# Optimization experiments

Measured on AMD Instinct MI355X. Metric: run time of the kernel, lower is better.

The kernel has to match this reference:

```python
import jax, jax.numpy as jnp
import numpy as np

N, E, B = 20000, 160000, 64
NFEAT, NHID, HEADS, NCLASS = 128, 64, 16, 10
GAT_SLOPE = 0.2    # LeakyReLU inside GATv2 attention
OUT_SLOPE = 0.01   # torch.nn.functional.leaky_relu default
TEMPERATURE = 1.0


def _lrelu(x, slope):
    return jnp.where(x >= 0, x, slope * x)


def gatv2_conv(x, src, dst, Wl, bl, Wr, br, att, bias):
    # x: [N, Fin]; PyG GATv2Conv with share_weights=False, concat=False (mean over heads)
    xl = (x @ Wl + bl).reshape(N, HEADS, NHID)   # source-side transform
    xr = (x @ Wr + br).reshape(N, HEADS, NHID)   # target-side transform
    e = _lrelu(xl[src] + xr[dst], GAT_SLOPE)     # [E', H, C] per-edge pre-activation
    logit = jnp.einsum('ehc,hc->eh', e, att)     # [E', H]
    # segment softmax over incoming edges of each target node (self-loops guarantee >=1 edge)
    m = jax.ops.segment_max(logit, dst, num_segments=N)
    m = jnp.where(jnp.isfinite(m), m, 0.0)
    ex = jnp.exp(logit - m[dst])
    den = jax.ops.segment_sum(ex, dst, num_segments=N)
    alpha = ex / den[dst]                        # [E', H]
    out = jax.ops.segment_sum(alpha[:, :, None] * xl[src], dst, num_segments=N)  # [N, H, C]
    return out.mean(axis=1) + bias               # concat=False -> head average, then bias


def setup_inputs() -> dict:
    key = jax.random.key(0)
    ks = jax.random.split(key, 20)
    s = 0.05
    inp = {
        'x': jax.random.normal(ks[0], (N, NFEAT), dtype=jnp.float32),
        'edge_index': jax.random.randint(ks[1], (2, E), 0, N, dtype=jnp.int64)
            if jax.config.jax_enable_x64 else jax.random.randint(ks[1], (2, E), 0, N).astype(jnp.int32),
        'batch': jnp.sort(jax.random.randint(ks[2], (N,), 0, B)).astype(jnp.int32),
        # GATv2 layer 1
        'W1l': jax.random.normal(ks[3], (NFEAT, HEADS * NHID), dtype=jnp.float32) * s,
        'b1l': jnp.zeros((HEADS * NHID,), jnp.float32),
        'W1r': jax.random.normal(ks[4], (NFEAT, HEADS * NHID), dtype=jnp.float32) * s,
        'b1r': jnp.zeros((HEADS * NHID,), jnp.float32),
        'att1': jax.random.normal(ks[5], (HEADS, NHID), dtype=jnp.float32) * s,
        'bias1': jnp.zeros((NHID,), jnp.float32),
        # GATv2 layer 2
        'W2l': jax.random.normal(ks[6], (NHID, HEADS * NHID), dtype=jnp.float32) * s,
        'b2l': jnp.zeros((HEADS * NHID,), jnp.float32),
        'W2r': jax.random.normal(ks[7], (NHID, HEADS * NHID), dtype=jnp.float32) * s,
        'b2r': jnp.zeros((HEADS * NHID,), jnp.float32),
        'att2': jax.random.normal(ks[8], (HEADS, NHID), dtype=jnp.float32) * s,
        'bias2': jnp.zeros((NHID,), jnp.float32),
        # heads
        'Wc': jax.random.normal(ks[9], (NHID, NCLASS), dtype=jnp.float32) * s,
        'bc': jnp.zeros((NCLASS,), jnp.float32),
        'Wv': jax.random.normal(ks[10], (NHID, 1), dtype=jnp.float32) * s,
        'bv': jnp.zeros((1,), jnp.float32),
    }
    return inp


def reference(x, edge_index, batch, W1l, b1l, W1r, b1r, att1, bias1,
              W2l, b2l, W2r, b2r, att2, bias2, Wc, bc, Wv, bv):
    loop = jnp.arange(N, dtype=edge_index.dtype)  # PyG add_self_loops=True
    src = jnp.concatenate([edge_index[0], loop])
    dst = jnp.concatenate([edge_index[1], loop])

    h = _lrelu(gatv2_conv(x, src, dst, W1l, b1l, W1r, b1r, att1, bias1), OUT_SLOPE)
    h = _lrelu(gatv2_conv(h, src, dst, W2l, b2l, W2r, b2r, att2, bias2), OUT_SLOPE)
    # dropout p=0.0 -> identity

    sums = jax.ops.segment_sum(h, batch, num_segments=B)           # [B, NHID]
    cnt = jax.ops.segment_sum(jnp.ones((N,), h.dtype), batch, num_segments=B)
    pooled = sums / jnp.maximum(cnt, 1.0)[:, None]                 # global_mean_pool

    logits = (pooled @ Wc + bc) / TEMPERATURE                      # [B, NCLASS]
    log_var = pooled @ Wv + bv                                     # [B, 1]
    return (logits, log_var)
```

## Files before the change

### kernel.cpp

```cpp
#include <hip/hip_runtime.h>
#include <hip/hip_bf16.h>
#include <hip/hip_fp16.h>
#include <math.h>

#define NN   20000
#define EE   160000
#define NBAT 64
#define NF   128
#define NH   64
#define NHEAD 16
#define NCLS 10
#define ETOT (EE + NN)

#define SCAN_BLK 1024
#define SCAN_NB  ((NN + SCAN_BLK - 1) / SCAN_BLK)

typedef __attribute__((ext_vector_type(8))) _Float16 half8;
typedef __attribute__((ext_vector_type(2))) _Float16 h2v;
typedef __attribute__((ext_vector_type(4))) float f32x4;
typedef unsigned short ushort_t;

#if __has_builtin(__builtin_amdgcn_fdot2)
typedef __fp16 fdot2_t __attribute__((ext_vector_type(2)));
static __device__ __forceinline__ float dot2(h2v a, h2v b, float c) {
    return __builtin_amdgcn_fdot2(__builtin_bit_cast(fdot2_t, a),
                                  __builtin_bit_cast(fdot2_t, b), c, false);
}
#else
static __device__ __forceinline__ float dot2(h2v a, h2v b, float c) {
    return c + (float)a.x * (float)b.x + (float)a.y * (float)b.y;
}
#endif

__global__ void k_hist_bounds(const int* __restrict__ ei, int* __restrict__ deg,
                              const int* __restrict__ batch, int* __restrict__ bstart) {
    int g = blockIdx.x * 256 + threadIdx.x;
    if (g < EE) atomicAdd(&deg[ei[EE + g]], 1);
    if (g < NN) {
        int b = batch[g];
        if (g == 0) for (int bb = 0; bb <= b; ++bb) bstart[bb] = 0;
        int bn = (g + 1 < NN) ? batch[g + 1] : NBAT;
        for (int bb = b + 1; bb <= bn; ++bb) bstart[bb] = g + 1;
    }
}

__global__ void k_scanA(const int* __restrict__ deg, int* __restrict__ incl,
                        int* __restrict__ bsum) {
    __shared__ int sh[SCAN_BLK];
    int t = threadIdx.x, idx = blockIdx.x * SCAN_BLK + t;
    int v = (idx < NN) ? deg[idx] : 0;
    sh[t] = v;
    __syncthreads();
    for (int off = 1; off < SCAN_BLK; off <<= 1) {
        int u = (t >= off) ? sh[t - off] : 0;
        __syncthreads();
        sh[t] += u;
        __syncthreads();
    }
    incl[idx] = sh[t];
    if (t == SCAN_BLK - 1) bsum[blockIdx.x] = sh[t];
}

__global__ void k_scanB(const int* __restrict__ bsum, int* __restrict__ boff,
                        int* __restrict__ rowptr) {
    if (threadIdx.x == 0) {
        int acc = 0;
        for (int b = 0; b < SCAN_NB; ++b) { boff[b] = acc; acc += bsum[b]; }
        rowptr[NN] = acc + NN;
    }
}

__global__ void k_scanC(const int* __restrict__ deg, const int* __restrict__ incl,
                        const int* __restrict__ boff, int* __restrict__ rowptr,
                        int* __restrict__ cursor, int* __restrict__ csr) {
    int idx = blockIdx.x * 256 + threadIdx.x;
    if (idx >= NN) return;
    int b = idx >> 10;
    int excl = boff[b] + incl[idx] - deg[idx];
    int base = excl + idx;
    rowptr[idx] = base;
    csr[base]   = idx;
    cursor[idx] = base + 1;
}

__global__ void k_scatter(const int* __restrict__ ei, int* __restrict__ cursor,
                          int* __restrict__ csr) {
    int e = blockIdx.x * 256 + threadIdx.x;
    if (e >= EE) return;
    int s = ei[e], d = ei[EE + e];
    int pos = atomicAdd(&cursor[d], 1);
    csr[pos] = s;
}

__global__ void k_split_w4(
    const float* __restrict__ W0, _Float16* __restrict__ T0,
    const float* __restrict__ W1, _Float16* __restrict__ T1,
    const float* __restrict__ W2, _Float16* __restrict__ T2,
    const float* __restrict__ W3, _Float16* __restrict__ T3)
{
    const int z = blockIdx.y;
    const float* W; _Float16* T; int K;
    if      (z == 0) { W = W0; T = T0; K = NF; }
    else if (z == 1) { W = W1; T = T1; K = NF; }
    else if (z == 2) { W = W2; T = T2; K = NH; }
    else             { W = W3; T = T3; K = NH; }
    int idx = blockIdx.x * 256 + threadIdx.x;
    if (idx >= K * 1024) return;
    int k = idx >> 10, n = idx & 1023;
    T[n * K + k] = (_Float16)W[idx];
}


template<int K>
__global__ __launch_bounds__(256) void k_gemm_l1(
    const float* __restrict__ X, int M,
    const _Float16* __restrict__ Wt0, const float* __restrict__ b0, _Float16* __restrict__ O0,
    const _Float16* __restrict__ Wt1, const float* __restrict__ b1, _Float16* __restrict__ O1)
{
    const _Float16* Wt = blockIdx.z ? Wt1 : Wt0;
    const float*    bi = blockIdx.z ? b1 : b0;
    _Float16*       O  = blockIdx.z ? O1 : O0;

    const int r0 = blockIdx.x * 128;
    const int c0 = blockIdx.y * 128;

    __shared__ __align__(16) ushort_t SH[128 * 128];
    char* AsB = (char*)SH;
    char* WsB = (char*)SH + 16384;

    const int t = threadIdx.x;
    const int lane = t & 63;
    const int wv = t >> 6, wr = wv >> 1, wc = wv & 1;
    const int fr = lane & 15;
    const int k0 = (lane >> 4) * 8;

    f32x4 acc[4][4] = {};

    for (int kt = 0; kt < K; kt += 64) {
        #pragma unroll
        for (int p = 0; p < 4; ++p) {
            int idx = p * 256 + t;
            int m  = idx >> 3;
            int kc = (idx & 7) * 8;
            int gr = r0 + m;
            half8 hv = {};
            if (gr < M) {
                float4 v0 = *(const float4*)(X + (size_t)gr * K + kt + kc);
                float4 v1 = *(const float4*)(X + (size_t)gr * K + kt + kc + 4);
                hv[0] = (_Float16)v0.x; hv[1] = (_Float16)v0.y;
                hv[2] = (_Float16)v0.z; hv[3] = (_Float16)v0.w;
                hv[4] = (_Float16)v1.x; hv[5] = (_Float16)v1.y;
                hv[6] = (_Float16)v1.z; hv[7] = (_Float16)v1.w;
            }
            int sw = (m * 128 + kc * 2) ^ ((m & 7) << 4);
            *(uint4*)(AsB + sw) = __builtin_bit_cast(uint4, hv);
            uint4 wv4 = *(const uint4*)(Wt + (size_t)(c0 + m) * K + kt + kc);
            *(uint4*)(WsB + sw) = wv4;
        }
        __syncthreads();

        #pragma unroll
        for (int ks = 0; ks < 64; ks += 32) {
            half8 a[4], b[4];
            #pragma unroll
            for (int i = 0; i < 4; ++i) {
                int row = wr * 64 + i * 16 + fr;
                int off = (row * 128 + (ks + k0) * 2) ^ ((row & 7) << 4);
                a[i] = *(const half8*)(AsB + off);
            }
            #pragma unroll
            for (int j = 0; j < 4; ++j) {
                int col = wc * 64 + j * 16 + fr;
                int off = (col * 128 + (ks + k0) * 2) ^ ((col & 7) << 4);
                b[j] = *(const half8*)(WsB + off);
            }
            #pragma unroll
            for (int i = 0; i < 4; ++i)
                #pragma unroll
                for (int j = 0; j < 4; ++j)
                    acc[i][j] = __builtin_amdgcn_mfma_f32_16x16x32_f16(a[i], b[j], acc[i][j], 0, 0, 0);
        }
        __syncthreads();
    }

    float bj[4];
    #pragma unroll
    for (int j = 0; j < 4; ++j) bj[j] = bi[c0 + wc * 64 + j * 16 + fr];
    #pragma unroll
    for (int i = 0; i < 4; ++i) {
        #pragma unroll
        for (int r = 0; r < 4; ++r) {
            int row_l = wr * 64 + i * 16 + (lane >> 4) * 4 + r;
            int s = ((row_l >> 2) & 7) << 4;
            #pragma unroll
            for (int j = 0; j < 4; ++j) {
                int col_l = wc * 64 + j * 16 + fr;
                *(_Float16*)((char*)SH + ((row_l * 256 + col_l * 2) ^ s)) =
                    (_Float16)(acc[i][j][r] + bj[j]);
            }
        }
    }
    __syncthreads();
    #pragma unroll
    for (int it = 0; it < 8; ++it) {
        int idx = it * 256 + t;
        int row_l = idx >> 4, c16 = idx & 15;
        int gr = r0 + row_l;
        if (gr < M) {
            int s = ((row_l >> 2) & 7) << 4;
            uint4 v = *(const uint4*)((char*)SH + ((row_l * 256 + c16 * 16) ^ s));
            *(uint4*)(O + (size_t)gr * 1024 + c0 + c16 * 8) = v;
        }
    }
}

template<int K>
__global__ __launch_bounds__(256) void k_gemm_l2(
    const _Float16* __restrict__ A, int M,
    const _Float16* __restrict__ Wt0, const float* __restrict__ b0, _Float16* __restrict__ O0,
    const _Float16* __restrict__ Wt1, const float* __restrict__ b1, _Float16* __restrict__ O1)
{
    const _Float16* Wt = blockIdx.z ? Wt1 : Wt0;
    const float*    bi = blockIdx.z ? b1 : b0;
    _Float16*       O  = blockIdx.z ? O1 : O0;

    const int r0 = blockIdx.x * 128;
    const int c0 = blockIdx.y * 128;

    __shared__ __align__(16) ushort_t SH[128 * 128];
    char* AsB = (char*)SH;
    char* WsB = (char*)SH + 16384;

    const int t = threadIdx.x;
    const int lane = t & 63;
    const int wv = t >> 6, wr = wv >> 1, wc = wv & 1;
    const int fr = lane & 15;
    const int k0 = (lane >> 4) * 8;

    f32x4 acc[4][4] = {};

    #pragma unroll
    for (int p = 0; p < 4; ++p) {
        int idx = p * 256 + t;
        int m  = idx >> 3;
        int kc = (idx & 7) * 8;
        int gr = r0 + m;
        uint4 av = make_uint4(0, 0, 0, 0);
        if (gr < M) av = *(const uint4*)(A + (size_t)gr * K + kc);
        int sw = (m * 128 + kc * 2) ^ ((m & 7) << 4);
        *(uint4*)(AsB + sw) = av;
        uint4 wv4 = *(const uint4*)(Wt + (size_t)(c0 + m) * K + kc);
        *(uint4*)(WsB + sw) = wv4;
    }
    __syncthreads();

    #pragma unroll
    for (int ks = 0; ks < 64; ks += 32) {
        half8 a[4], b[4];
        #pragma unroll
        for (int i = 0; i < 4; ++i) {
            int row = wr * 64 + i * 16 + fr;
            int off = (row * 128 + (ks + k0) * 2) ^ ((row & 7) << 4);
            a[i] = *(const half8*)(AsB + off);
        }
        #pragma unroll
        for (int j = 0; j < 4; ++j) {
            int col = wc * 64 + j * 16 + fr;
            int off = (col * 128 + (ks + k0) * 2) ^ ((col & 7) << 4);
            b[j] = *(const half8*)(WsB + off);
        }
        #pragma unroll
        for (int i = 0; i < 4; ++i)
            #pragma unroll
            for (int j = 0; j < 4; ++j)
                acc[i][j] = __builtin_amdgcn_mfma_f32_16x16x32_f16(a[i], b[j], acc[i][j], 0, 0, 0);
    }
    __syncthreads();

    float bj[4];
    #pragma unroll
    for (int j = 0; j < 4; ++j) bj[j] = bi[c0 + wc * 64 + j * 16 + fr];
    #pragma unroll
    for (int i = 0; i < 4; ++i) {
        #pragma unroll
        for (int r = 0; r < 4; ++r) {
            int row_l = wr * 64 + i * 16 + (lane >> 4) * 4 + r;
            int s = ((row_l >> 2) & 7) << 4;
            #pragma unroll
            for (int j = 0; j < 4; ++j) {
                int col_l = wc * 64 + j * 16 + fr;
                *(_Float16*)((char*)SH + ((row_l * 256 + col_l * 2) ^ s)) =
                    (_Float16)(acc[i][j][r] + bj[j]);
            }
        }
    }
    __syncthreads();
    #pragma unroll
    for (int it = 0; it < 8; ++it) {
        int idx = it * 256 + t;
        int row_l = idx >> 4, c16 = idx & 15;
        int gr = r0 + row_l;
        if (gr < M) {
            int s = ((row_l >> 2) & 7) << 4;
            uint4 v = *(const uint4*)((char*)SH + ((row_l * 256 + c16 * 16) ^ s));
            *(uint4*)(O + (size_t)gr * 1024 + c0 + c16 * 8) = v;
        }
    }
}

static __device__ __forceinline__ float logit8(
    half8 a0, half8 a1, half8 xr0, half8 xr1, const h2v* att2)
{
    half8 t0 = a0 + xr0;
    half8 t1 = a1 + xr1;
    t0 = __builtin_elementwise_max(t0, t0 * (_Float16)0.2f);
    t1 = __builtin_elementwise_max(t1, t1 * (_Float16)0.2f);
    const h2v* p0 = (const h2v*)&t0;
    const h2v* p1 = (const h2v*)&t1;
    float lg = 0.f;
    #pragma unroll
    for (int j = 0; j < 4; ++j) lg = dot2(p0[j], att2[j], lg);
    #pragma unroll
    for (int j = 0; j < 4; ++j) lg = dot2(p1[j], att2[4 + j], lg);
    return lg;
}

__global__ __launch_bounds__(256) void k_attn(
    const _Float16* __restrict__ xl, const _Float16* __restrict__ xr,
    const float* __restrict__ att, const float* __restrict__ bias,
    const int* __restrict__ rowptr, const int* __restrict__ csr,
    _Float16* __restrict__ hout)
{
    const int wave = threadIdx.x >> 6;
    const int lane = threadIdx.x & 63;
    const int n = blockIdx.x * 4 + wave;
    if (n >= NN) return;
    const int h  = lane >> 2;
    const int cc = lane & 3;
    const int cb = h * NH + cc * 16;

    h2v att2[8];
    #pragma unroll
    for (int i = 0; i < 4; ++i) {
        float4 a = *(const float4*)(att + cb + i * 4);
        att2[i * 2 + 0] = h2v{(_Float16)a.x, (_Float16)a.y};
        att2[i * 2 + 1] = h2v{(_Float16)a.z, (_Float16)a.w};
    }
    const half8 xr0 = *(const half8*)(xr + (size_t)n * 1024 + cb);
    const half8 xr1 = *(const half8*)(xr + (size_t)n * 1024 + cb + 8);

    float acc[16];
    #pragma unroll
    for (int j = 0; j < 16; ++j) acc[j] = 0.f;
    float den = 0.f;

    const int e0 = rowptr[n], e1 = rowptr[n + 1];
    for (int e = e0; e < e1; e += 4) {
        int src[4];
        #pragma unroll
        for (int j = 0; j < 4; ++j) {
            int ee = e + j;
            src[j] = csr[(ee < e1) ? ee : (e1 - 1)];
        }
        half8 xa0[4], xa1[4];
        #pragma unroll
        for (int j = 0; j < 4; ++j) {
            const _Float16* p = xl + (size_t)src[j] * 1024 + cb;
            xa0[j] = *(const half8*)p;
            xa1[j] = *(const half8*)(p + 8);
        }
        #pragma unroll
        for (int j = 0; j < 4; ++j) {
            float lg = logit8(xa0[j], xa1[j], xr0, xr1, att2);
            lg += __shfl_xor(lg, 1);
            lg += __shfl_xor(lg, 2);
            float p = (e + j < e1) ? __expf(lg) : 0.f;
            den += p;
            const _Float16* va = (const _Float16*)&xa0[j];
            const _Float16* vb = (const _Float16*)&xa1[j];
            #pragma unroll
            for (int q = 0; q < 8; ++q) acc[q]     = fmaf((float)va[q], p, acc[q]);
            #pragma unroll
            for (int q = 0; q < 8; ++q) acc[8 + q] = fmaf((float)vb[q], p, acc[8 + q]);
        }
    }

    const float inv = 1.f / den;
    float v[16];
    #pragma unroll
    for (int j = 0; j < 16; ++j) v[j] = acc[j] * inv;
    #pragma unroll
    for (int mask = 4; mask <= 32; mask <<= 1)
        #pragma unroll
        for (int j = 0; j < 16; ++j) v[j] += __shfl_xor(v[j], mask);

    if (h == 0) {
        float bvv[16];
        #pragma unroll
        for (int i = 0; i < 4; ++i)
            *(float4*)(bvv + i * 4) = *(const float4*)(bias + cc * 16 + i * 4);
        half8 o0, o1;
        #pragma unroll
        for (int j = 0; j < 8; ++j) {
            float t0 = v[j] * 0.0625f + bvv[j];
            float t1 = v[8 + j] * 0.0625f + bvv[8 + j];
            o0[j] = (_Float16)fmaxf(t0, 0.01f * t0);
            o1[j] = (_Float16)fmaxf(t1, 0.01f * t1);
        }
        *(half8*)(hout + (size_t)n * NH + cc * 16)     = o0;
        *(half8*)(hout + (size_t)n * NH + cc * 16 + 8) = o1;
    }
}

__global__ __launch_bounds__(256) void k_pool_heads(
    const _Float16* __restrict__ h2buf, const int* __restrict__ bstart,
    const float* __restrict__ Wc, const float* __restrict__ bc,
    const float* __restrict__ Wv, const float* __restrict__ bv,
    float* __restrict__ out)
{
    const int b = blockIdx.x;
    const int c = threadIdx.x & 63, r = threadIdx.x >> 6;
    const int s = bstart[b], e = bstart[b + 1];
    float sum = 0.f;
    for (int n = s + r; n < e; n += 4)
        sum += (float)h2buf[(size_t)n * NH + c];
    __shared__ float red[4][NH];
    red[r][c] = sum;
    __syncthreads();
    if (r == 0)
        red[0][c] = (red[0][c] + red[1][c] + red[2][c] + red[3][c]) /
                    fmaxf((float)(e - s), 1.f);
    __syncthreads();
    if (threadIdx.x < NCLS) {
        float a = bc[threadIdx.x];
        for (int k = 0; k < NH; ++k) a = fmaf(red[0][k], Wc[k * NCLS + threadIdx.x], a);
        out[b * NCLS + threadIdx.x] = a;
    } else if (threadIdx.x == NCLS) {
        float a = bv[0];
        for (int k = 0; k < NH; ++k) a = fmaf(red[0][k], Wv[k], a);
        out[NBAT * NCLS + b] = a;
    }
}

extern "C" void kernel_launch(void* const* d_in, const int* in_sizes, int n_in,
                              void* d_out, int out_size, void* d_ws, size_t ws_size,
                              hipStream_t stream)
{
    const float* x     = (const float*)d_in[0];
    const int*   ei    = (const int*)  d_in[1];
    const int*   batch = (const int*)  d_in[2];
    const float* W1l = (const float*)d_in[3],  *b1l = (const float*)d_in[4];
    const float* W1r = (const float*)d_in[5],  *b1r = (const float*)d_in[6];
    const float* att1 = (const float*)d_in[7], *bias1 = (const float*)d_in[8];
    const float* W2l = (const float*)d_in[9],  *b2l = (const float*)d_in[10];
    const float* W2r = (const float*)d_in[11], *b2r = (const float*)d_in[12];
    const float* att2 = (const float*)d_in[13], *bias2 = (const float*)d_in[14];
    const float* Wc = (const float*)d_in[15],  *bc = (const float*)d_in[16];
    const float* Wv = (const float*)d_in[17],  *bv = (const float*)d_in[18];
    float* out = (float*)d_out;

    char* ws = (char*)d_ws;
    size_t off = 0;
    auto carve = [&](size_t bytes) {
        char* p = ws + off;
        off = (off + bytes + 255) & ~(size_t)255;
        return p;
    };
    _Float16* xl    = (_Float16*)carve((size_t)NN * 1024 * 2);
    _Float16* xr    = (_Float16*)carve((size_t)NN * 1024 * 2);
    _Float16* h2f   = (_Float16*)carve((size_t)NN * NH * 2);
    _Float16* h1    = (_Float16*)carve((size_t)NN * NH * 2);
    _Float16* Wt1l  = (_Float16*)carve((size_t)1024 * NF * 2);
    _Float16* Wt1r  = (_Float16*)carve((size_t)1024 * NF * 2);
    _Float16* Wt2l  = (_Float16*)carve((size_t)1024 * NH * 2);
    _Float16* Wt2r  = (_Float16*)carve((size_t)1024 * NH * 2);
    int*      deg    = (int*)carve((size_t)NN * 4);
    int*      incl   = (int*)carve((size_t)SCAN_NB * SCAN_BLK * 4);
    int*      bsum   = (int*)carve((size_t)SCAN_NB * 4);
    int*      boff   = (int*)carve((size_t)SCAN_NB * 4);
    int*      cursor = (int*)carve((size_t)NN * 4);
    int*      rowptr = (int*)carve((size_t)(NN + 1) * 4);
    int*      csr    = (int*)carve((size_t)ETOT * 4);
    int*      bstart = (int*)carve((size_t)(NBAT + 1) * 4);

    hipMemsetAsync(deg, 0, (size_t)NN * 4, stream);

    k_hist_bounds<<<(EE + 255) / 256, 256, 0, stream>>>(ei, deg, batch, bstart);
    k_scanA<<<SCAN_NB, SCAN_BLK, 0, stream>>>(deg, incl, bsum);
    k_scanB<<<1, 64, 0, stream>>>(bsum, boff, rowptr);
    k_scanC<<<(NN + 255) / 256, 256, 0, stream>>>(deg, incl, boff, rowptr, cursor, csr);
    k_scatter<<<(EE + 255) / 256, 256, 0, stream>>>(ei, cursor, csr);

    k_split_w4<<<dim3((NF * 1024 + 255) / 256, 4), 256, 0, stream>>>(
        W1l, Wt1l, W1r, Wt1r, W2l, Wt2l, W2r, Wt2r);

    const int MB = (NN + 127) / 128;
    k_gemm_l1<NF><<<dim3(MB, 8, 2), 256, 0, stream>>>(
        x, NN, Wt1l, b1l, xl, Wt1r, b1r, xr);
    k_attn<<<NN / 4, 256, 0, stream>>>(xl, xr, att1, bias1, rowptr, csr, h1);
    k_gemm_l2<NH><<<dim3(MB, 8, 2), 256, 0, stream>>>(
        h1, NN, Wt2l, b2l, xl, Wt2r, b2r, xr);
    k_attn<<<NN / 4, 256, 0, stream>>>(xl, xr, att2, bias2, rowptr, csr, h2f);
    k_pool_heads<<<NBAT, 256, 0, stream>>>(h2f, bstart, Wc, bc, Wv, bv, out);
}
```

Before: 333.3 us.

## Fuse CSR build preprocessing into fewer kernels with atomic block offsets

Merges the degree histogram, batch bounds, and weight transpose/convert into one launch. The three-kernel scan becomes a single scan kernel that takes each block's base from a global atomic counter, so CSR segments can land in arbitrary block order. Attention now reads a row start plus degree instead of rowptr and runs 1024-thread blocks with 16 nodes each. This cuts several tiny launches and serial dependencies, but gives up the ordered CSR layout, which may hurt locality, and the larger blocks may change occupancy.

```diff
diff --git a/kernel.cpp b/kernel.cpp
--- a/kernel.cpp
+++ b/kernel.cpp
@@ -12,8 +12,10 @@
 #define NCLS 10
 #define ETOT (EE + NN)
 
-#define SCAN_BLK 1024
-#define SCAN_NB  ((NN + SCAN_BLK - 1) / SCAN_BLK)
+#define P2_BLK 1024
+#define P2_NB  ((NN + P2_BLK - 1) / P2_BLK)
+#define WELEMS (2 * NF * 1024 + 2 * NH * 1024)
+#define PRE1_TOT (EE + NN + WELEMS)
 
 typedef __attribute__((ext_vector_type(8))) _Float16 half8;
 typedef __attribute__((ext_vector_type(2))) _Float16 h2v;
@@ -32,55 +34,65 @@
 }
 #endif
 
-__global__ void k_hist_bounds(const int* __restrict__ ei, int* __restrict__ deg,
-                              const int* __restrict__ batch, int* __restrict__ bstart) {
+__global__ void k_pre1(
+    const int* __restrict__ ei, int* __restrict__ deg,
+    const int* __restrict__ batch, int* __restrict__ bstart,
+    const float* __restrict__ W1l, _Float16* __restrict__ Wt1l,
+    const float* __restrict__ W1r, _Float16* __restrict__ Wt1r,
+    const float* __restrict__ W2l, _Float16* __restrict__ Wt2l,
+    const float* __restrict__ W2r, _Float16* __restrict__ Wt2r)
+{
     int g = blockIdx.x * 256 + threadIdx.x;
-    if (g < EE) atomicAdd(&deg[ei[EE + g]], 1);
-    if (g < NN) {
-        int b = batch[g];
-        if (g == 0) for (int bb = 0; bb <= b; ++bb) bstart[bb] = 0;
-        int bn = (g + 1 < NN) ? batch[g + 1] : NBAT;
-        for (int bb = b + 1; bb <= bn; ++bb) bstart[bb] = g + 1;
-    }
-}
-
-__global__ void k_scanA(const int* __restrict__ deg, int* __restrict__ incl,
-                        int* __restrict__ bsum) {
-    __shared__ int sh[SCAN_BLK];
-    int t = threadIdx.x, idx = blockIdx.x * SCAN_BLK + t;
-    int v = (idx < NN) ? deg[idx] : 0;
-    sh[t] = v;
-    __syncthreads();
-    for (int off = 1; off < SCAN_BLK; off <<= 1) {
+    if (g < EE) {
+        atomicAdd(&deg[ei[EE + g]], 1);
+    } else if (g < EE + NN) {
+        int n = g - EE;
+        int b = batch[n];
+        if (n == 0) for (int bb = 0; bb <= b; ++bb) bstart[bb] = 0;
+        int bn = (n + 1 < NN) ? batch[n + 1] : NBAT;
+        for (int bb = b + 1; bb <= bn; ++bb) bstart[bb] = n + 1;
+    } else if (g < PRE1_TOT) {
+        int w = g - (EE + NN);
+        const float* W; _Float16* T; int K, local;
+        if      (w < NF * 1024)            { W = W1l; T = Wt1l; K = NF; local = w; }
+        else if (w < 2 * NF * 1024)        { W = W1r; T = Wt1r; K = NF; local = w - NF * 1024; }
+        else if (w < 2 * NF * 1024 + NH * 1024)
+                                           { W = W2l; T = Wt2l; K = NH; local = w - 2 * NF * 1024; }
+        else                               { W = W2r; T = Wt2r; K = NH; local = w - 2 * NF * 1024 - NH * 1024; }
+        int k = local >> 10, n = local & 1023;
+        T[n * K + k] = (_Float16)W[local];
+    }
+}
+
+__global__ __launch_bounds__(1024) void k_pre2(
+    const int* __restrict__ deg, int* __restrict__ gcur,
+    int* __restrict__ rowstart, int* __restrict__ cursor, int* __restrict__ csr)
+{
+    __shared__ int sh[P2_BLK];
+    __shared__ int base_sh;
+    int t = threadIdx.x;
+    int idx = blockIdx.x * P2_BLK + t;
+    int d = (idx < NN) ? deg[idx] : 0;
+    sh[t] = d;
+    __syncthreads();
+    for (int off = 1; off < P2_BLK; off <<= 1) {
         int u = (t >= off) ? sh[t - off] : 0;
         __syncthreads();
         sh[t] += u;
         __syncthreads();
     }
-    incl[idx] = sh[t];
-    if (t == SCAN_BLK - 1) bsum[blockIdx.x] = sh[t];
-}
-
-__global__ void k_scanB(const int* __restrict__ bsum, int* __restrict__ boff,
-                        int* __restrict__ rowptr) {
-    if (threadIdx.x == 0) {
-        int acc = 0;
-        for (int b = 0; b < SCAN_NB; ++b) { boff[b] = acc; acc += bsum[b]; }
-        rowptr[NN] = acc + NN;
-    }
-}
-
-__global__ void k_scanC(const int* __restrict__ deg, const int* __restrict__ incl,
-                        const int* __restrict__ boff, int* __restrict__ rowptr,
-                        int* __restrict__ cursor, int* __restrict__ csr) {
-    int idx = blockIdx.x * 256 + threadIdx.x;
-    if (idx >= NN) return;
-    int b = idx >> 10;
-    int excl = boff[b] + incl[idx] - deg[idx];
-    int base = excl + idx;
-    rowptr[idx] = base;
-    csr[base]   = idx;
-    cursor[idx] = base + 1;
+    if (t == P2_BLK - 1) {
+        int nvalid = NN - blockIdx.x * P2_BLK;
+        if (nvalid > P2_BLK) nvalid = P2_BLK;
+        base_sh = atomicAdd(gcur, sh[t] + nvalid);
+    }
+    __syncthreads();
+    if (idx < NN) {
+        int base = base_sh + (sh[t] - d) + t;
+        rowstart[idx] = base;
+        csr[base]     = idx;
+        cursor[idx]   = base + 1;
+    }
 }
 
 __global__ void k_scatter(const int* __restrict__ ei, int* __restrict__ cursor,
@@ -90,24 +102,6 @@
     int s = ei[e], d = ei[EE + e];
     int pos = atomicAdd(&cursor[d], 1);
     csr[pos] = s;
-}
-
-__global__ void k_split_w4(
-    const float* __restrict__ W0, _Float16* __restrict__ T0,
-    const float* __restrict__ W1, _Float16* __restrict__ T1,
-    const float* __restrict__ W2, _Float16* __restrict__ T2,
-    const float* __restrict__ W3, _Float16* __restrict__ T3)
-{
-    const int z = blockIdx.y;
-    const float* W; _Float16* T; int K;
-    if      (z == 0) { W = W0; T = T0; K = NF; }
-    else if (z == 1) { W = W1; T = T1; K = NF; }
-    else if (z == 2) { W = W2; T = T2; K = NH; }
-    else             { W = W3; T = T3; K = NH; }
-    int idx = blockIdx.x * 256 + threadIdx.x;
-    if (idx >= K * 1024) return;
-    int k = idx >> 10, n = idx & 1023;
-    T[n * K + k] = (_Float16)W[idx];
 }
 
 
@@ -325,15 +319,15 @@
     return lg;
 }
 
-__global__ __launch_bounds__(256) void k_attn(
+__global__ __launch_bounds__(1024) void k_attn(
     const _Float16* __restrict__ xl, const _Float16* __restrict__ xr,
     const float* __restrict__ att, const float* __restrict__ bias,
-    const int* __restrict__ rowptr, const int* __restrict__ csr,
-    _Float16* __restrict__ hout)
+    const int* __restrict__ rowstart, const int* __restrict__ deg,
+    const int* __restrict__ csr, _Float16* __restrict__ hout)
 {
     const int wave = threadIdx.x >> 6;
     const int lane = threadIdx.x & 63;
-    const int n = blockIdx.x * 4 + wave;
+    const int n = blockIdx.x * 16 + wave;
     if (n >= NN) return;
     const int h  = lane >> 2;
     const int cc = lane & 3;
@@ -354,7 +348,7 @@
     for (int j = 0; j < 16; ++j) acc[j] = 0.f;
     float den = 0.f;
 
-    const int e0 = rowptr[n], e1 = rowptr[n + 1];
+    const int e0 = rowstart[n], e1 = e0 + deg[n] + 1;
     for (int e = e0; e < e1; e += 4) {
         int src[4];
         #pragma unroll
@@ -474,32 +468,29 @@
     _Float16* Wt1r  = (_Float16*)carve((size_t)1024 * NF * 2);
     _Float16* Wt2l  = (_Float16*)carve((size_t)1024 * NH * 2);
     _Float16* Wt2r  = (_Float16*)carve((size_t)1024 * NH * 2);
-    int*      deg    = (int*)carve((size_t)NN * 4);
-    int*      incl   = (int*)carve((size_t)SCAN_NB * SCAN_BLK * 4);
-    int*      bsum   = (int*)carve((size_t)SCAN_NB * 4);
-    int*      boff   = (int*)carve((size_t)SCAN_NB * 4);
-    int*      cursor = (int*)carve((size_t)NN * 4);
-    int*      rowptr = (int*)carve((size_t)(NN + 1) * 4);
-    int*      csr    = (int*)carve((size_t)ETOT * 4);
-    int*      bstart = (int*)carve((size_t)(NBAT + 1) * 4);
-
-    hipMemsetAsync(deg, 0, (size_t)NN * 4, stream);
-
-    k_hist_bounds<<<(EE + 255) / 256, 256, 0, stream>>>(ei, deg, batch, bstart);
-    k_scanA<<<SCAN_NB, SCAN_BLK, 0, stream>>>(deg, incl, bsum);
-    k_scanB<<<1, 64, 0, stream>>>(bsum, boff, rowptr);
-    k_scanC<<<(NN + 255) / 256, 256, 0, stream>>>(deg, incl, boff, rowptr, cursor, csr);
+    int*      deg     = (int*)carve((size_t)(NN + 1) * 4);
+    int*      gcur    = deg + NN;
+    int*      rowstart= (int*)carve((size_t)NN * 4);
+    int*      cursor  = (int*)carve((size_t)NN * 4);
+    int*      csr     = (int*)carve((size_t)ETOT * 4);
+    int*      bstart  = (int*)carve((size_t)(NBAT + 1) * 4);
+
+    hipMemsetAsync(deg, 0, (size_t)(NN + 1) * 4, stream);
+
+    k_pre1<<<(PRE1_TOT + 255) / 256, 256, 0, stream>>>(
+        ei, deg, batch, bstart,
+        W1l, Wt1l, W1r, Wt1r, W2l, Wt2l, W2r, Wt2r);
+    k_pre2<<<P2_NB, P2_BLK, 0, stream>>>(deg, gcur, rowstart, cursor, csr);
     k_scatter<<<(EE + 255) / 256, 256, 0, stream>>>(ei, cursor, csr);
-
-    k_split_w4<<<dim3((NF * 1024 + 255) / 256, 4), 256, 0, stream>>>(
-        W1l, Wt1l, W1r, Wt1r, W2l, Wt2l, W2r, Wt2r);
 
     const int MB = (NN + 127) / 128;
     k_gemm_l1<NF><<<dim3(MB, 8, 2), 256, 0, stream>>>(
         x, NN, Wt1l, b1l, xl, Wt1r, b1r, xr);
-    k_attn<<<NN / 4, 256, 0, stream>>>(xl, xr, att1, bias1, rowptr, csr, h1);
+    k_attn<<<(NN + 15) / 16, 1024, 0, stream>>>(xl, xr, att1, bias1,
+                                                rowstart, deg, csr, h1);
     k_gemm_l2<NH><<<dim3(MB, 8, 2), 256, 0, stream>>>(
         h1, NN, Wt2l, b2l, xl, Wt2r, b2r, xr);
-    k_attn<<<NN / 4, 256, 0, stream>>>(xl, xr, att2, bias2, rowptr, csr, h2f);
+    k_attn<<<(NN + 15) / 16, 1024, 0, stream>>>(xl, xr, att2, bias2,
+                                                rowstart, deg, csr, h2f);
     k_pool_heads<<<NBAT, 256, 0, stream>>>(h2f, bstart, Wc, bc, Wv, bv, out);
 }
```

After: 353.5 us. 1.06x slower.
